# Optimization experiments

Hardware: AMD Instinct MI355X
Metric: run time of the kernel (lower is better)

Reference implementation:

```python
import jax, jax.numpy as jnp
import numpy as np

EMB_DIM = 256
ATT_DIM = 256
B, S = 8, 2048


def setup_inputs() -> dict:
    key = jax.random.key(0)
    ks = jax.random.split(key, 9)
    scale = 1.0 / np.sqrt(EMB_DIM)
    inp = {
        "x": jax.random.normal(ks[0], (B, S, EMB_DIM), dtype=jnp.float32),
        "mask": jax.random.randint(ks[1], (B, S, S), 0, 2, dtype=jnp.int32),
        "Wq": jax.random.uniform(ks[2], (EMB_DIM, ATT_DIM), jnp.float32, -scale, scale),
        "bq": jax.random.uniform(ks[3], (ATT_DIM,), jnp.float32, -scale, scale),
        "Wk": jax.random.uniform(ks[4], (EMB_DIM, ATT_DIM), jnp.float32, -scale, scale),
        "bk": jax.random.uniform(ks[5], (ATT_DIM,), jnp.float32, -scale, scale),
        "Wv": jax.random.uniform(ks[6], (EMB_DIM, ATT_DIM), jnp.float32, -scale, scale),
        "bv": jax.random.uniform(ks[7], (ATT_DIM,), jnp.float32, -scale, scale),
    }
    return inp


def reference(x, mask, Wq, bq, Wk, bk, Wv, bv):
    # Linear projections: (B,S,E) @ (E,A) + (A,)
    q = jnp.einsum("bse,ea->bsa", x, Wq) + bq
    k = jnp.einsum("bse,ea->bsa", x, Wk) + bk
    v = jnp.einsum("bse,ea->bsa", x, Wv) + bv
    # scores: (B,S,S)
    scores = jnp.einsum("bqa,bka->bqk", q, k) / jnp.sqrt(jnp.float32(ATT_DIM))
    scores = jnp.where(mask == 0, jnp.float32(-1e9), scores)
    attn = jax.nn.softmax(scores, axis=-1)
    return jnp.einsum("bqk,bka->bqa", attn, v)
```

## Files before the change

kernel.cpp:

```cpp
#include <hip/hip_runtime.h>
#include <hip/hip_bf16.h>
#include <stdint.h>

#define BATCH 8
#define SEQ   2048
#define EMB   256
#define ADIM  256

typedef __bf16 bf16_t;
typedef __attribute__((ext_vector_type(8))) __bf16 bf16x8;
typedef __attribute__((ext_vector_type(4))) float  f32x4;
typedef uint32_t u32;
typedef __attribute__((ext_vector_type(4))) u32 u32x4;
typedef long long i64;

static __device__ __forceinline__ f32x4 mfma16(bf16x8 a, bf16x8 b, f32x4 c) {
    return __builtin_amdgcn_mfma_f32_16x16x32_bf16(a, b, c, 0, 0, 0);
}

static __device__ __forceinline__ void gld16(const void* g, void* l) {
    __builtin_amdgcn_global_load_lds((const __attribute__((address_space(1))) u32*)g,
                                     (__attribute__((address_space(3))) u32*)l, 16, 0, 0);
}

__global__ __launch_bounds__(256) void wtkv_kernel(const float* __restrict__ Wk,
                                                   const float* __restrict__ Wv,
                                                   bf16_t* __restrict__ wt) {
    int tid = blockIdx.x * 256 + threadIdx.x;
    int m = tid >> 16;
    int i = tid & 65535;
    int a = i >> 8, e = i & 255;
    const float* W = (m == 0) ? Wk : Wv;
    wt[m * 65536 + a * 256 + e] = (bf16_t)W[e * 256 + a];
}

__global__ __launch_bounds__(256) void maskbits_kernel(const u32* __restrict__ mask,
                                                       u32* __restrict__ bitw) {
    int idx = blockIdx.x * 256 + threadIdx.x;
    const u32* mp = mask + (size_t)idx * 32;
    u32 wd = 0;
    #pragma unroll
    for (int q = 0; q < 8; ++q) {
        u32x4 v = *(const u32x4*)(mp + q * 4);
        #pragma unroll
        for (int j = 0; j < 4; ++j)
            wd |= (v[j] ? 1u : 0u) << (q * 4 + j);
    }
    bitw[idx] = wd;
}

__global__ __launch_bounds__(128, 1) void proj_kv(const float* __restrict__ x,
                                                  const bf16_t* __restrict__ wt,
                                                  const float* __restrict__ bk,
                                                  const float* __restrict__ bv,
                                                  char* __restrict__ Ksw,
                                                  char* __restrict__ Vsw) {
    __shared__ __align__(16) char stg[2][10240];
    const int tid  = threadIdx.x;
    const int wid  = tid >> 6;
    const int lane = tid & 63;
    const int lq   = lane >> 4;
    const int ln   = lane & 15;
    const int blk  = blockIdx.x;
    const int b    = blk >> 6;
    const int tile = blk & 63;
    const int mbase = blk * 32 + wid * 16;
    char* S = stg[wid];

    bf16x8 xf[8];
    const float* xp = x + (size_t)(mbase + ln) * EMB;
    #pragma unroll
    for (int c = 0; c < 8; ++c) {
        f32x4 a0 = *(const f32x4*)(xp + c * 32 + lq * 8);
        f32x4 a1 = *(const f32x4*)(xp + c * 32 + lq * 8 + 4);
        bf16x8 v;
        v[0] = (bf16_t)a0[0]; v[1] = (bf16_t)a0[1]; v[2] = (bf16_t)a0[2]; v[3] = (bf16_t)a0[3];
        v[4] = (bf16_t)a1[0]; v[5] = (bf16_t)a1[1]; v[6] = (bf16_t)a1[2]; v[7] = (bf16_t)a1[3];
        xf[c] = v;
    }

    f32x4 acc[16];

    #pragma unroll
    for (int t = 0; t < 16; ++t) acc[t] = (f32x4){0.f, 0.f, 0.f, 0.f};
    {
        const bf16_t* w = wt;
        #pragma unroll
        for (int c = 0; c < 8; ++c)
            #pragma unroll
            for (int t = 0; t < 16; ++t) {
                bf16x8 wf = *(const bf16x8*)(w + (size_t)(t * 16 + ln) * 256 + c * 32 + lq * 8);
                acc[t] = mfma16(xf[c], wf, acc[t]);
            }
    }
    #pragma unroll
    for (int t = 0; t < 16; ++t) {
        float bb = bk[t * 16 + ln];
        #pragma unroll
        for (int r = 0; r < 4; ++r)
            *(bf16_t*)(S + (lq * 4 + r) * 512 + (t * 16 + ln) * 2) = (bf16_t)(acc[t][r] + bb);
    }
    asm volatile("s_waitcnt lgkmcnt(0)" ::: "memory");
    {
        char* Kg = Ksw + (size_t)b * 1048576 + (size_t)tile * 16384 + wid * 8192;
        const int rh = lane >> 5;
        const int p  = lane & 31;
        #pragma unroll
        for (int i = 0; i < 8; ++i) {
            int row = i * 2 + rh;
            int n   = wid * 16 + row;
            int cb  = p ^ (n & 7);
            f32x4 ch = *(const f32x4*)(S + row * 512 + cb * 16);
            *(f32x4*)(Kg + row * 512 + p * 16) = ch;
        }
    }

    #pragma unroll
    for (int t = 0; t < 16; ++t) acc[t] = (f32x4){0.f, 0.f, 0.f, 0.f};
    {
        const bf16_t* w = wt + 65536;
        #pragma unroll
        for (int c = 0; c < 8; ++c)
            #pragma unroll
            for (int t = 0; t < 16; ++t) {
                bf16x8 wf = *(const bf16x8*)(w + (size_t)(t * 16 + ln) * 256 + c * 32 + lq * 8);
                acc[t] = mfma16(xf[c], wf, acc[t]);
            }
    }
    #pragma unroll
    for (int t = 0; t < 16; ++t) {
        float bb = bv[t * 16 + ln];
        #pragma unroll
        for (int r = 0; r < 4; ++r)
            *(bf16_t*)(S + (t * 16 + ln) * 40 + (lq * 4 + r) * 2) = (bf16_t)(acc[t][r] + bb);
    }
    asm volatile("s_waitcnt lgkmcnt(0)" ::: "memory");
    {
        char* Vg = Vsw + (size_t)b * 1048576 + (size_t)tile * 16384;
        const int half = lane & 1;
        const int kq   = wid * 2 + half;
        #pragma unroll
        for (int i = 0; i < 8; ++i) {
            int a   = i * 32 + (lane >> 1);
            int pos = kq ^ (a & 3) ^ ((a >> 2) & 3);
            f32x4 ch = *(const f32x4*)(S + a * 40 + half * 16);
            *(f32x4*)(Vg + a * 64 + pos * 16) = ch;
        }
    }
}

__global__ __launch_bounds__(256, 2) void flash_kernel(const float* __restrict__ x,
                                                       const float* __restrict__ WqM,
                                                       const float* __restrict__ bq,
                                                       const char* __restrict__ Ksw,
                                                       const char* __restrict__ Vsw,
                                                       const int* __restrict__ mask,
                                                       const u32* __restrict__ bitw,
                                                       float* __restrict__ lp,
                                                       i64 bs, i64 rs, i64 ks,
                                                       float* __restrict__ out) {
    __shared__ __align__(16) char smem[71168];
    const int tid  = threadIdx.x;
    const int wid  = tid >> 6;
    const int lane = tid & 63;
    const int lq   = lane >> 4;
    const int ln   = lane & 15;
    const int qw   = wid >> 1;
    const int kw   = wid & 1;
    const int batch = blockIdx.x & 7;
    const int kvh   = (blockIdx.x >> 3) & 1;
    const int qbase = (blockIdx.x >> 4) * 64;

    const char* Kb = Ksw + (size_t)batch * 1048576 + (size_t)(kvh * 32) * 16384;
    const char* Vb = Vsw + (size_t)batch * 1048576 + (size_t)(kvh * 32) * 16384;
    char*  Pq_ = smem + 65536 + qw * 2560;
    char*  Pt  = smem + 65536 + wid * 1280;
    float* Ls  = (float*)(smem + 70656);

    const char* kg0 = Kb + wid * 4096 + lane * 16;
    const char* vg0 = Vb + wid * 4096 + lane * 16;

    const int* mroot = mask + (size_t)batch * SEQ * SEQ +
                       (size_t)(qbase + qw * 32) * SEQ + kvh * 1024 + kw * 16 + ln;
    const u32* broot = bitw ? bitw + (size_t)batch * 131072 +
                              (size_t)(qbase + qw * 32) * 64 + kvh * 32
                            : nullptr;
    const int bitpos = kw * 16 + ln;

    {
        char* kl = smem + wid * 4096;
        char* vl = smem + 16384 + wid * 4096;
        #pragma unroll
        for (int i = 0; i < 4; ++i) gld16(kg0 + i * 1024, kl + i * 1024);
        #pragma unroll
        for (int i = 0; i < 4; ++i) gld16(vg0 + i * 1024, vl + i * 1024);
    }
    asm volatile("" ::: "memory");
    int mv[2][2][4];
    if (broot) {
        #pragma unroll
        for (int w = 0; w < 2; ++w)
            #pragma unroll
            for (int h = 0; h < 2; ++h)
                #pragma unroll
                for (int r = 0; r < 4; ++r)
                    mv[w][h][r] = (int)((broot[(h * 16 + lq * 4 + r) * 64 + w] >> bitpos) & 1u);
    } else {
        #pragma unroll
        for (int w = 0; w < 2; ++w)
            #pragma unroll
            for (int h = 0; h < 2; ++h)
                #pragma unroll
                for (int r = 0; r < 4; ++r)
                    mv[w][h][r] = mroot[(size_t)(h * 16 + lq * 4 + r) * SEQ + w * 32];
    }

    bf16x8 qf[2][8];
    {
        bf16x8 xf[2][8];
        #pragma unroll
        for (int h = 0; h < 2; ++h) {
            const float* xp = x + (size_t)(batch * SEQ + qbase + qw * 32 + h * 16 + ln) * EMB;
            #pragma unroll
            for (int c = 0; c < 8; ++c) {
                f32x4 a = *(const f32x4*)(xp + c * 32 + lq * 8);
                f32x4 b = *(const f32x4*)(xp + c * 32 + lq * 8 + 4);
                bf16x8 v;
                v[0] = (bf16_t)a[0]; v[1] = (bf16_t)a[1]; v[2] = (bf16_t)a[2]; v[3] = (bf16_t)a[3];
                v[4] = (bf16_t)b[0]; v[5] = (bf16_t)b[1]; v[6] = (bf16_t)b[2]; v[7] = (bf16_t)b[3];
                xf[h][c] = v;
            }
        }
        f32x4 qacc[2][16];
        #pragma unroll
        for (int h = 0; h < 2; ++h)
            #pragma unroll
            for (int t = 0; t < 16; ++t) qacc[h][t] = (f32x4){0.f, 0.f, 0.f, 0.f};

        char* Wsp = smem + 32768;
        const int e = ln & 7;
        #pragma unroll 1
        for (int cp = 0; cp < 8; ++cp) {
            __syncthreads();
            const float* wqp = WqM + (size_t)(cp * 32) * 256 + tid;
            #pragma unroll
            for (int i = 0; i < 4; ++i) {
                bf16x8 pk;
                #pragma unroll
                for (int j = 0; j < 8; ++j)
                    pk[j] = (bf16_t)wqp[(size_t)(i * 8 + j) * 256];
                *(bf16x8*)(Wsp + tid * 128 + ((i ^ (tid & 7)) * 16)) = pk;
            }
            __syncthreads();
            #pragma unroll
            for (int t = 0; t < 16; ++t) {
                bf16x8 wf = *(const bf16x8*)(Wsp + (t * 16 + ln) * 128 + ((lq ^ e) * 16));
                qacc[0][t] = mfma16(xf[0][cp], wf, qacc[0][t]);
                qacc[1][t] = mfma16(xf[1][cp], wf, qacc[1][t]);
            }
        }
        #pragma unroll
        for (int h = 0; h < 2; ++h) {
            #pragma unroll
            for (int c = 0; c < 8; ++c) {
                #pragma unroll
                for (int half2 = 0; half2 < 2; ++half2) {
                    int t = 2 * c + half2;
                    float bb = bq[t * 16 + ln];
                    #pragma unroll
                    for (int r = 0; r < 4; ++r) {
                        float v = (qacc[h][t][r] + bb) * 0.0625f;
                        ((bf16_t*)(Pt + (lq * 4 + r) * 80))[half2 * 16 + ln] = (bf16_t)v;
                    }
                }
                qf[h][c] = *(const bf16x8*)(Pt + ln * 80 + lq * 16);
            }
        }
    }

    f32x4 o[2][8];
    #pragma unroll
    for (int h = 0; h < 2; ++h)
        #pragma unroll
        for (int t = 0; t < 8; ++t) o[h][t] = (f32x4){0.f, 0.f, 0.f, 0.f};
    float lsum[2][4] = {{0.f,0.f,0.f,0.f},{0.f,0.f,0.f,0.f}};

    const int kswz = ln & 7;
    const int vswz = (lq ^ (ln & 3) ^ ((ln >> 2) & 3)) * 16;
    const int n0   = kw * 16 + ln;

    for (int kt = 0; kt < 32; ++kt) {
        asm volatile("s_waitcnt vmcnt(8) lgkmcnt(0)\n\ts_barrier" ::: "memory");
        if (kt + 1 < 32) {
            int nb = (kt + 1) & 1;
            const char* kg = kg0 + (size_t)(kt + 1) * 16384;
            const char* vg = vg0 + (size_t)(kt + 1) * 16384;
            char* kl = smem + nb * 32768 + wid * 4096;
            char* vl = smem + nb * 32768 + 16384 + wid * 4096;
            #pragma unroll
            for (int i = 0; i < 4; ++i) gld16(kg + i * 1024, kl + i * 1024);
            #pragma unroll
            for (int i = 0; i < 4; ++i) gld16(vg + i * 1024, vl + i * 1024);
        }
        const int buf = kt & 1;
        const char* Ksb = smem + buf * 32768;
        const char* Vsb = smem + buf * 32768 + 16384;

        f32x4 s0 = (f32x4){0.f,0.f,0.f,0.f};
        f32x4 s1 = (f32x4){0.f,0.f,0.f,0.f};
        const char* krow = Ksb + n0 * 512;
        #pragma unroll
        for (int c = 0; c < 8; ++c) {
            bf16x8 kf = *(const bf16x8*)(krow + (((c * 4 + lq) ^ kswz) * 16));
            s0 = mfma16(qf[0][c], kf, s0);
            s1 = mfma16(qf[1][c], kf, s1);
        }

        const int (*mc)[4] = mv[kt & 1];
        #pragma unroll
        for (int r = 0; r < 4; ++r) {
            float p0 = mc[0][r] ? __expf(s0[r]) : 0.f;
            float p1 = mc[1][r] ? __expf(s1[r]) : 0.f;
            lsum[0][r] += p0;
            lsum[1][r] += p1;
            ((bf16_t*)(Pq_ + (lq * 4 + r) * 80))[kw * 16 + ln]      = (bf16_t)p0;
            ((bf16_t*)(Pq_ + (16 + lq * 4 + r) * 80))[kw * 16 + ln] = (bf16_t)p1;
        }

        asm volatile("s_waitcnt lgkmcnt(0)\n\ts_barrier" ::: "memory");

        {
            const int ktn = (kt + 2 < 32) ? kt + 2 : 31;
            int (*md)[4] = mv[kt & 1];
            if (broot) {
                #pragma unroll
                for (int h = 0; h < 2; ++h)
                    #pragma unroll
                    for (int r = 0; r < 4; ++r)
                        md[h][r] = (int)((broot[(h * 16 + lq * 4 + r) * 64 + ktn] >> bitpos) & 1u);
            } else {
                #pragma unroll
                for (int h = 0; h < 2; ++h)
                    #pragma unroll
                    for (int r = 0; r < 4; ++r)
                        md[h][r] = mroot[(size_t)(h * 16 + lq * 4 + r) * SEQ + ktn * 32];
            }
        }

        bf16x8 pa0 = *(const bf16x8*)(Pq_ + ln * 80 + lq * 16);
        bf16x8 pa1 = *(const bf16x8*)(Pq_ + (16 + ln) * 80 + lq * 16);

        const char* vbase = Vsb + (kw * 128 + ln) * 64 + vswz;
        #pragma unroll
        for (int t = 0; t < 8; ++t) {
            bf16x8 vf = *(const bf16x8*)(vbase + t * 1024);
            o[0][t] = mfma16(pa0, vf, o[0][t]);
            o[1][t] = mfma16(pa1, vf, o[1][t]);
        }
    }

    __syncthreads();
    #pragma unroll
    for (int h = 0; h < 2; ++h) {
        #pragma unroll
        for (int r = 0; r < 4; ++r) {
            float v = lsum[h][r];
            v += __shfl_xor(v, 1);
            v += __shfl_xor(v, 2);
            v += __shfl_xor(v, 4);
            v += __shfl_xor(v, 8);
            if (ln == 0) Ls[(qw * 2 + kw) * 32 + h * 16 + lq * 4 + r] = v;
            lsum[h][r] = v;
        }
    }
    __syncthreads();

    if (kw == 0 && ln == 0) {
        #pragma unroll
        for (int h = 0; h < 2; ++h)
            #pragma unroll
            for (int r = 0; r < 4; ++r) {
                int row = h * 16 + lq * 4 + r;
                float tot = lsum[h][r] + Ls[(qw * 2 + 1) * 32 + row];
                lp[bs * batch + rs * (qbase + qw * 32 + row) + ks * kvh] = tot;
            }
    }

    #pragma unroll
    for (int h = 0; h < 2; ++h) {
        #pragma unroll
        for (int r = 0; r < 4; ++r) {
            float* orow = out + (size_t)(batch * SEQ + qbase + qw * 32 + h * 16 + lq * 4 + r) * ADIM
                          + kw * 128 + ln;
            #pragma unroll
            for (int t = 0; t < 8; ++t)
                atomicAdd(orow + t * 16, o[h][t][r]);
        }
    }
}

__global__ __launch_bounds__(256) void merge_kernel(const float* __restrict__ lp,
                                                    i64 bs, i64 rs, i64 ks,
                                                    float* __restrict__ out) {
    int idx  = blockIdx.x * 256 + threadIdx.x;
    int base = idx * 4;
    int row  = base >> 8;
    int b = row >> 11, r = row & 2047;
    float l0 = lp[bs * b + rs * r];
    float l1 = lp[bs * b + rs * r + ks];
    float inv = 1.0f / (l0 + l1);
    f32x4 v = *(const f32x4*)(out + base);
    v[0] *= inv; v[1] *= inv; v[2] *= inv; v[3] *= inv;
    *(f32x4*)(out + base) = v;
}

extern "C" void kernel_launch(void* const* d_in, const int* in_sizes, int n_in,
                              void* d_out, int out_size, void* d_ws, size_t ws_size,
                              hipStream_t stream) {
    const float* x    = (const float*)d_in[0];
    int*         mask = (int*)d_in[1];
    const float* Wq   = (const float*)d_in[2];
    const float* bq   = (const float*)d_in[3];
    const float* Wk   = (const float*)d_in[4];
    const float* bk   = (const float*)d_in[5];
    const float* Wv   = (const float*)d_in[6];
    const float* bv   = (const float*)d_in[7];
    float* out = (float*)d_out;

    char* Ksw = (char*)d_ws;
    char* Vsw = Ksw + (size_t)8 * 1024 * 1024;
    bf16_t* wt = (bf16_t*)d_out;

    const size_t MB = 1024 * 1024;
    const size_t lsum_bytes = (size_t)2 * BATCH * SEQ * sizeof(float);
    u32*   bitw = nullptr;
    float* lp; i64 bs, rs, ks;
    if (ws_size >= 20 * MB + lsum_bytes) {
        bitw = (u32*)(Ksw + 16 * MB);
        lp = (float*)(Ksw + 20 * MB);
        bs = (i64)2 * SEQ;  rs = 2;  ks = 1;
    } else if (ws_size >= 16 * MB + lsum_bytes) {
        lp = (float*)(Ksw + 16 * MB);
        bs = (i64)2 * SEQ;  rs = 2;  ks = 1;
    } else {
        lp = (float*)mask;
        bs = (i64)SEQ * SEQ;  rs = SEQ;  ks = 1024;
    }

    wtkv_kernel<<<512, 256, 0, stream>>>(Wk, Wv, wt);
    if (bitw) maskbits_kernel<<<4096, 256, 0, stream>>>((const u32*)mask, bitw);
    proj_kv<<<512, 128, 0, stream>>>(x, wt, bk, bv, Ksw, Vsw);
    hipMemsetAsync(d_out, 0, (size_t)out_size * sizeof(float), stream);
    flash_kernel<<<512, 256, 0, stream>>>(x, Wq, bq, Ksw, Vsw, mask, bitw,
                                          lp, bs, rs, ks, out);
    merge_kernel<<<4096, 256, 0, stream>>>(lp, bs, rs, ks, out);
}
```

Baseline: 367.1 us.

## Split flash kernel work across 8 waves with 16 query rows each

```diff
diff --git a/kernel.cpp b/kernel.cpp
--- a/kernel.cpp
+++ b/kernel.cpp
@@ -149,7 +149,7 @@
     }
 }
 
-__global__ __launch_bounds__(256, 2) void flash_kernel(const float* __restrict__ x,
+__global__ __launch_bounds__(512, 4) void flash_kernel(const float* __restrict__ x,
                                                        const float* __restrict__ WqM,
                                                        const float* __restrict__ bq,
                                                        const char* __restrict__ Ksw,
@@ -159,7 +159,7 @@
                                                        float* __restrict__ lp,
                                                        i64 bs, i64 rs, i64 ks,
                                                        float* __restrict__ out) {
-    __shared__ __align__(16) char smem[71168];
+    __shared__ __align__(16) char smem[76288];
     const int tid  = threadIdx.x;
     const int wid  = tid >> 6;
     const int lane = tid & 63;
@@ -173,54 +173,47 @@
 
     const char* Kb = Ksw + (size_t)batch * 1048576 + (size_t)(kvh * 32) * 16384;
     const char* Vb = Vsw + (size_t)batch * 1048576 + (size_t)(kvh * 32) * 16384;
-    char*  Pq_ = smem + 65536 + qw * 2560;
+    char*  Pq_ = smem + 65536 + qw * 1280;
     char*  Pt  = smem + 65536 + wid * 1280;
-    float* Ls  = (float*)(smem + 70656);
-
-    const char* kg0 = Kb + wid * 4096 + lane * 16;
-    const char* vg0 = Vb + wid * 4096 + lane * 16;
+    float* Ls  = (float*)(smem + 75776);
+
+    const int dhalf = wid >> 2, dqr = wid & 3;
+    const char* gsrc0 = (dhalf ? Vb : Kb) + dqr * 4096 + lane * 16;
+    const int   ldst0 = dhalf * 16384 + dqr * 4096;
 
     const int* mroot = mask + (size_t)batch * SEQ * SEQ +
-                       (size_t)(qbase + qw * 32) * SEQ + kvh * 1024 + kw * 16 + ln;
+                       (size_t)(qbase + qw * 16) * SEQ + kvh * 1024 + kw * 16 + ln;
     const u32* broot = bitw ? bitw + (size_t)batch * 131072 +
-                              (size_t)(qbase + qw * 32) * 64 + kvh * 32
+                              (size_t)(qbase + qw * 16) * 64 + kvh * 32
                             : nullptr;
     const int bitpos = kw * 16 + ln;
 
     {
-        char* kl = smem + wid * 4096;
-        char* vl = smem + 16384 + wid * 4096;
-        #pragma unroll
-        for (int i = 0; i < 4; ++i) gld16(kg0 + i * 1024, kl + i * 1024);
-        #pragma unroll
-        for (int i = 0; i < 4; ++i) gld16(vg0 + i * 1024, vl + i * 1024);
+        char* dl = smem + ldst0;
+        #pragma unroll
+        for (int i = 0; i < 4; ++i) gld16(gsrc0 + i * 1024, dl + i * 1024);
     }
     asm volatile("" ::: "memory");
-    int mv[2][2][4];
+    int mv[2][4];
     if (broot) {
         #pragma unroll
         for (int w = 0; w < 2; ++w)
             #pragma unroll
-            for (int h = 0; h < 2; ++h)
-                #pragma unroll
-                for (int r = 0; r < 4; ++r)
-                    mv[w][h][r] = (int)((broot[(h * 16 + lq * 4 + r) * 64 + w] >> bitpos) & 1u);
+            for (int r = 0; r < 4; ++r)
+                mv[w][r] = (int)((broot[(lq * 4 + r) * 64 + w] >> bitpos) & 1u);
     } else {
         #pragma unroll
         for (int w = 0; w < 2; ++w)
             #pragma unroll
-            for (int h = 0; h < 2; ++h)
-                #pragma unroll
-                for (int r = 0; r < 4; ++r)
-                    mv[w][h][r] = mroot[(size_t)(h * 16 + lq * 4 + r) * SEQ + w * 32];
-    }
-
-    bf16x8 qf[2][8];
-    {
-        bf16x8 xf[2][8];
-        #pragma unroll
-        for (int h = 0; h < 2; ++h) {
-            const float* xp = x + (size_t)(batch * SEQ + qbase + qw * 32 + h * 16 + ln) * EMB;
+            for (int r = 0; r < 4; ++r)
+                mv[w][r] = mroot[(size_t)(lq * 4 + r) * SEQ + w * 32];
+    }
+
+    bf16x8 qf[8];
+    {
+        bf16x8 xf[8];
+        {
+            const float* xp = x + (size_t)(batch * SEQ + qbase + qw * 16 + ln) * EMB;
             #pragma unroll
             for (int c = 0; c < 8; ++c) {
                 f32x4 a = *(const f32x4*)(xp + c * 32 + lq * 8);
@@ -228,174 +221,144 @@
                 bf16x8 v;
                 v[0] = (bf16_t)a[0]; v[1] = (bf16_t)a[1]; v[2] = (bf16_t)a[2]; v[3] = (bf16_t)a[3];
                 v[4] = (bf16_t)b[0]; v[5] = (bf16_t)b[1]; v[6] = (bf16_t)b[2]; v[7] = (bf16_t)b[3];
-                xf[h][c] = v;
-            }
-        }
-        f32x4 qacc[2][16];
-        #pragma unroll
-        for (int h = 0; h < 2; ++h)
-            #pragma unroll
-            for (int t = 0; t < 16; ++t) qacc[h][t] = (f32x4){0.f, 0.f, 0.f, 0.f};
+                xf[c] = v;
+            }
+        }
+        f32x4 qacc[16];
+        #pragma unroll
+        for (int t = 0; t < 16; ++t) qacc[t] = (f32x4){0.f, 0.f, 0.f, 0.f};
 
         char* Wsp = smem + 32768;
-        const int e = ln & 7;
+        const int grp = tid >> 8;
+        const int aa  = tid & 255;
+        const int e   = ln & 7;
         #pragma unroll 1
         for (int cp = 0; cp < 8; ++cp) {
             __syncthreads();
-            const float* wqp = WqM + (size_t)(cp * 32) * 256 + tid;
-            #pragma unroll
-            for (int i = 0; i < 4; ++i) {
+            const float* wqp = WqM + (size_t)(cp * 32) * 256 + aa;
+            #pragma unroll
+            for (int i = 0; i < 2; ++i) {
+                int ip = grp * 2 + i;
                 bf16x8 pk;
                 #pragma unroll
                 for (int j = 0; j < 8; ++j)
-                    pk[j] = (bf16_t)wqp[(size_t)(i * 8 + j) * 256];
-                *(bf16x8*)(Wsp + tid * 128 + ((i ^ (tid & 7)) * 16)) = pk;
+                    pk[j] = (bf16_t)wqp[(size_t)(ip * 8 + j) * 256];
+                *(bf16x8*)(Wsp + aa * 128 + ((ip ^ (aa & 7)) * 16)) = pk;
             }
             __syncthreads();
             #pragma unroll
             for (int t = 0; t < 16; ++t) {
                 bf16x8 wf = *(const bf16x8*)(Wsp + (t * 16 + ln) * 128 + ((lq ^ e) * 16));
-                qacc[0][t] = mfma16(xf[0][cp], wf, qacc[0][t]);
-                qacc[1][t] = mfma16(xf[1][cp], wf, qacc[1][t]);
-            }
-        }
-        #pragma unroll
-        for (int h = 0; h < 2; ++h) {
-            #pragma unroll
-            for (int c = 0; c < 8; ++c) {
+                qacc[t] = mfma16(xf[cp], wf, qacc[t]);
+            }
+        }
+        #pragma unroll
+        for (int c = 0; c < 8; ++c) {
+            #pragma unroll
+            for (int half2 = 0; half2 < 2; ++half2) {
+                int t = 2 * c + half2;
+                float bb = bq[t * 16 + ln];
                 #pragma unroll
-                for (int half2 = 0; half2 < 2; ++half2) {
-                    int t = 2 * c + half2;
-                    float bb = bq[t * 16 + ln];
-                    #pragma unroll
-                    for (int r = 0; r < 4; ++r) {
-                        float v = (qacc[h][t][r] + bb) * 0.0625f;
-                        ((bf16_t*)(Pt + (lq * 4 + r) * 80))[half2 * 16 + ln] = (bf16_t)v;
-                    }
+                for (int r = 0; r < 4; ++r) {
+                    float v = (qacc[t][r] + bb) * 0.0625f;
+                    ((bf16_t*)(Pt + (lq * 4 + r) * 80))[half2 * 16 + ln] = (bf16_t)v;
                 }
-                qf[h][c] = *(const bf16x8*)(Pt + ln * 80 + lq * 16);
-            }
-        }
-    }
-
-    f32x4 o[2][8];
-    #pragma unroll
-    for (int h = 0; h < 2; ++h)
-        #pragma unroll
-        for (int t = 0; t < 8; ++t) o[h][t] = (f32x4){0.f, 0.f, 0.f, 0.f};
-    float lsum[2][4] = {{0.f,0.f,0.f,0.f},{0.f,0.f,0.f,0.f}};
+            }
+            qf[c] = *(const bf16x8*)(Pt + ln * 80 + lq * 16);
+        }
+    }
+
+    f32x4 o[8];
+    #pragma unroll
+    for (int t = 0; t < 8; ++t) o[t] = (f32x4){0.f, 0.f, 0.f, 0.f};
+    float lsum[4] = {0.f, 0.f, 0.f, 0.f};
 
     const int kswz = ln & 7;
     const int vswz = (lq ^ (ln & 3) ^ ((ln >> 2) & 3)) * 16;
     const int n0   = kw * 16 + ln;
 
     for (int kt = 0; kt < 32; ++kt) {
-        asm volatile("s_waitcnt vmcnt(8) lgkmcnt(0)\n\ts_barrier" ::: "memory");
+        asm volatile("s_waitcnt vmcnt(4) lgkmcnt(0)\n\ts_barrier" ::: "memory");
         if (kt + 1 < 32) {
-            int nb = (kt + 1) & 1;
-            const char* kg = kg0 + (size_t)(kt + 1) * 16384;
-            const char* vg = vg0 + (size_t)(kt + 1) * 16384;
-            char* kl = smem + nb * 32768 + wid * 4096;
-            char* vl = smem + nb * 32768 + 16384 + wid * 4096;
-            #pragma unroll
-            for (int i = 0; i < 4; ++i) gld16(kg + i * 1024, kl + i * 1024);
-            #pragma unroll
-            for (int i = 0; i < 4; ++i) gld16(vg + i * 1024, vl + i * 1024);
-        }
-        const int buf = kt & 1;
-        const char* Ksb = smem + buf * 32768;
-        const char* Vsb = smem + buf * 32768 + 16384;
-
-        f32x4 s0 = (f32x4){0.f,0.f,0.f,0.f};
-        f32x4 s1 = (f32x4){0.f,0.f,0.f,0.f};
+            const char* gs = gsrc0 + (size_t)(kt + 1) * 16384;
+            char* dl = smem + ((kt + 1) & 1) * 32768 + ldst0;
+            #pragma unroll
+            for (int i = 0; i < 4; ++i) gld16(gs + i * 1024, dl + i * 1024);
+        }
+        const char* Ksb = smem + (kt & 1) * 32768;
+        const char* Vsb = Ksb + 16384;
+
+        f32x4 s0 = (f32x4){0.f, 0.f, 0.f, 0.f};
         const char* krow = Ksb + n0 * 512;
         #pragma unroll
         for (int c = 0; c < 8; ++c) {
             bf16x8 kf = *(const bf16x8*)(krow + (((c * 4 + lq) ^ kswz) * 16));
-            s0 = mfma16(qf[0][c], kf, s0);
-            s1 = mfma16(qf[1][c], kf, s1);
-        }
-
-        const int (*mc)[4] = mv[kt & 1];
+            s0 = mfma16(qf[c], kf, s0);
+        }
+
+        const int* mc = mv[kt & 1];
         #pragma unroll
         for (int r = 0; r < 4; ++r) {
-            float p0 = mc[0][r] ? __expf(s0[r]) : 0.f;
-            float p1 = mc[1][r] ? __expf(s1[r]) : 0.f;
-            lsum[0][r] += p0;
-            lsum[1][r] += p1;
-            ((bf16_t*)(Pq_ + (lq * 4 + r) * 80))[kw * 16 + ln]      = (bf16_t)p0;
-            ((bf16_t*)(Pq_ + (16 + lq * 4 + r) * 80))[kw * 16 + ln] = (bf16_t)p1;
+            float p0 = mc[r] ? __expf(s0[r]) : 0.f;
+            lsum[r] += p0;
+            ((bf16_t*)(Pq_ + (lq * 4 + r) * 80))[kw * 16 + ln] = (bf16_t)p0;
         }
 
         asm volatile("s_waitcnt lgkmcnt(0)\n\ts_barrier" ::: "memory");
 
         {
             const int ktn = (kt + 2 < 32) ? kt + 2 : 31;
-            int (*md)[4] = mv[kt & 1];
+            int* md = mv[kt & 1];
             if (broot) {
                 #pragma unroll
-                for (int h = 0; h < 2; ++h)
-                    #pragma unroll
-                    for (int r = 0; r < 4; ++r)
-                        md[h][r] = (int)((broot[(h * 16 + lq * 4 + r) * 64 + ktn] >> bitpos) & 1u);
+                for (int r = 0; r < 4; ++r)
+                    md[r] = (int)((broot[(lq * 4 + r) * 64 + ktn] >> bitpos) & 1u);
             } else {
                 #pragma unroll
-                for (int h = 0; h < 2; ++h)
-                    #pragma unroll
-                    for (int r = 0; r < 4; ++r)
-                        md[h][r] = mroot[(size_t)(h * 16 + lq * 4 + r) * SEQ + ktn * 32];
+                for (int r = 0; r < 4; ++r)
+                    md[r] = mroot[(size_t)(lq * 4 + r) * SEQ + ktn * 32];
             }
         }
 
         bf16x8 pa0 = *(const bf16x8*)(Pq_ + ln * 80 + lq * 16);
-        bf16x8 pa1 = *(const bf16x8*)(Pq_ + (16 + ln) * 80 + lq * 16);
 
         const char* vbase = Vsb + (kw * 128 + ln) * 64 + vswz;
         #pragma unroll
         for (int t = 0; t < 8; ++t) {
             bf16x8 vf = *(const bf16x8*)(vbase + t * 1024);
-            o[0][t] = mfma16(pa0, vf, o[0][t]);
-            o[1][t] = mfma16(pa1, vf, o[1][t]);
+            o[t] = mfma16(pa0, vf, o[t]);
         }
     }
 
     __syncthreads();
     #pragma unroll
-    for (int h = 0; h < 2; ++h) {
+    for (int r = 0; r < 4; ++r) {
+        float v = lsum[r];
+        v += __shfl_xor(v, 1);
+        v += __shfl_xor(v, 2);
+        v += __shfl_xor(v, 4);
+        v += __shfl_xor(v, 8);
+        if (ln == 0) Ls[(qw * 2 + kw) * 16 + lq * 4 + r] = v;
+        lsum[r] = v;
+    }
+    __syncthreads();
+
+    if (kw == 0 && ln == 0) {
         #pragma unroll
         for (int r = 0; r < 4; ++r) {
-            float v = lsum[h][r];
-            v += __shfl_xor(v, 1);
-            v += __shfl_xor(v, 2);
-            v += __shfl_xor(v, 4);
-            v += __shfl_xor(v, 8);
-            if (ln == 0) Ls[(qw * 2 + kw) * 32 + h * 16 + lq * 4 + r] = v;
-            lsum[h][r] = v;
-        }
-    }
-    __syncthreads();
-
-    if (kw == 0 && ln == 0) {
-        #pragma unroll
-        for (int h = 0; h < 2; ++h)
-            #pragma unroll
-            for (int r = 0; r < 4; ++r) {
-                int row = h * 16 + lq * 4 + r;
-                float tot = lsum[h][r] + Ls[(qw * 2 + 1) * 32 + row];
-                lp[bs * batch + rs * (qbase + qw * 32 + row) + ks * kvh] = tot;
-            }
-    }
-
-    #pragma unroll
-    for (int h = 0; h < 2; ++h) {
-        #pragma unroll
-        for (int r = 0; r < 4; ++r) {
-            float* orow = out + (size_t)(batch * SEQ + qbase + qw * 32 + h * 16 + lq * 4 + r) * ADIM
-                          + kw * 128 + ln;
-            #pragma unroll
-            for (int t = 0; t < 8; ++t)
-                atomicAdd(orow + t * 16, o[h][t][r]);
-        }
+            int row = lq * 4 + r;
+            float tot = lsum[r] + Ls[(qw * 2 + 1) * 16 + row];
+            lp[bs * batch + rs * (qbase + qw * 16 + row) + ks * kvh] = tot;
+        }
+    }
+
+    #pragma unroll
+    for (int r = 0; r < 4; ++r) {
+        float* orow = out + (size_t)(batch * SEQ + qbase + qw * 16 + lq * 4 + r) * ADIM
+                      + kw * 128 + ln;
+        #pragma unroll
+        for (int t = 0; t < 8; ++t)
+            atomicAdd(orow + t * 16, o[t][r]);
     }
 }
 
@@ -451,7 +414,7 @@
     if (bitw) maskbits_kernel<<<4096, 256, 0, stream>>>((const u32*)mask, bitw);
     proj_kv<<<512, 128, 0, stream>>>(x, wt, bk, bv, Ksw, Vsw);
     hipMemsetAsync(d_out, 0, (size_t)out_size * sizeof(float), stream);
-    flash_kernel<<<512, 256, 0, stream>>>(x, Wq, bq, Ksw, Vsw, mask, bitw,
+    flash_kernel<<<512, 512, 0, stream>>>(x, Wq, bq, Ksw, Vsw, mask, bitw,
                                           lp, bs, rs, ks, out);
     merge_kernel<<<4096, 256, 0, stream>>>(lp, bs, rs, ks, out);
 }
```

Result: slower. 379.5 us (+3.4%).
